# Optimization experiments

Measured on AMD Instinct MI355X. Metric: run time of the kernel, lower is better.

## Reference

```python
import jax, jax.numpy as jnp
import numpy as np

B_, L_, DIN, DM, DS, DR, K = 2, 1024, 1024, 2048, 16, 128, 4


def setup_inputs() -> dict:
    key = jax.random.key(0)
    ks = jax.random.split(key, 10)
    s = lambda k, shape, sc=0.02: (jax.random.normal(k, shape, jnp.float32) * sc)
    A_init = jnp.tile(jnp.arange(1, DS + 1, dtype=jnp.float32)[None, :], (DM, 1))  # (DM, DS)
    return {
        'x_in': jax.random.normal(ks[0], (B_, L_, DIN), jnp.float32),
        'W_in': s(ks[1], (DIN, DM)),
        'W_res': s(ks[2], (DIN, DM)),
        'W_out': s(ks[3], (DM, DIN)),
        'conv_w': s(ks[4], (DM, K), 0.1),   # depthwise conv weight (torch shape (DM,1,K) squeezed)
        'conv_b': jnp.zeros((DM,), jnp.float32),
        'A_log': jnp.log(A_init),
        'D': jnp.ones((DM,), jnp.float32),
        'W_B': s(ks[5], (DM, DS)),
        'W_C': s(ks[6], (DM, DS)),
        'W_dt': s(ks[7], (DM, DR)),
        'dt_w': s(ks[8], (DR, DM)),
        'dt_b': jnp.zeros((DM,), jnp.float32),
    }


def reference(x_in, W_in, W_res, W_out, conv_w, conv_b, A_log, D, W_B, W_C, W_dt, dt_w, dt_b):
    Bb, L, _ = x_in.shape
    x = x_in @ W_in                     # (B, L, DM)
    res = x_in @ W_res                  # (B, L, DM)
    # Causal depthwise conv1d: pad left k-1, truncate to L (matches Conv1d(padding=k-1)[:, :, :L])
    xp = jnp.pad(x, ((0, 0), (K - 1, 0), (0, 0)))
    xc = conv_b
    for i in range(K):
        xc = xc + xp[:, i:i + L, :] * conv_w[:, i]
    xc = jax.nn.silu(xc)                # (B, L, DM)
    # Selective SSM (fused_ssm)
    A = -jnp.exp(A_log)                 # (DM, DS)
    Bp = xc @ W_B                       # (B, L, DS)
    Cp = xc @ W_C                       # (B, L, DS)
    delta = jax.nn.softplus((xc @ W_dt) @ dt_w + dt_b)  # (B, L, DM)
    dA = jnp.exp(delta[..., None] * A)                       # (B, L, DM, DS)
    dBu = delta[..., None] * Bp[:, :, None, :] * xc[..., None]  # (B, L, DM, DS)

    def step(h, inp):
        dA_t, dBu_t, C_t = inp
        h = dA_t * h + dBu_t                         # (B, DM, DS)
        y = jnp.einsum('bdn,bn->bd', h, C_t)         # (B, DM)
        return h, y

    h0 = jnp.zeros((Bb, DM, DS), jnp.float32)
    _, ys = jax.lax.scan(step, h0, (dA.transpose(1, 0, 2, 3), dBu.transpose(1, 0, 2, 3), Cp.transpose(1, 0, 2)))
    y = ys.transpose(1, 0, 2) + D * xc  # (B, L, DM)
    y = y * jax.nn.silu(res)
    return y @ W_out                    # (B, L, DIN)
```

## Files before the change

### kernel.cpp

```cpp
#include <hip/hip_runtime.h>
#include <hip/hip_bf16.h>

constexpr int B_  = 2;
constexpr int L_  = 1024;
constexpr int DIN = 1024;
constexpr int DM  = 2048;
constexpr int DS  = 16;
constexpr int DR  = 128;
constexpr int KC  = 4;
constexpr int M_  = B_ * L_;
constexpr int NP2 = 256;
constexpr int KSLICES = 8;
constexpr int KSL = DM / KSLICES;

constexpr int NC = 64;
constexpr int CL = L_ / NC;
constexpr int S_ = B_ * DM * DS;

typedef __bf16 bf16x8 __attribute__((ext_vector_type(8)));
typedef float  f32x4  __attribute__((ext_vector_type(4)));

__device__ __forceinline__ void gload_lds16(const void* g, void* l) {
    __builtin_amdgcn_global_load_lds(
        (const __attribute__((address_space(1))) void*)g,
        (__attribute__((address_space(3))) void*)l, 16, 0, 0);
}

__device__ __forceinline__ void transpose_block(const float* __restrict__ in,
                                                __bf16* __restrict__ out,
                                                int R, int C, int bx, int by, int t) {
    __shared__ float tile[32][33];
    int tx = t & 31, ty = t >> 5;
    #pragma unroll
    for (int j = 0; j < 32; j += 8)
        tile[ty + j][tx] = in[(size_t)(by * 32 + ty + j) * C + (bx * 32 + tx)];
    __syncthreads();
    #pragma unroll
    for (int j = 0; j < 32; j += 8)
        out[(size_t)(bx * 32 + ty + j) * R + (by * 32 + tx)] = (__bf16)tile[tx][ty + j];
}

__global__ void prep_all(const float* __restrict__ x_in, const float* __restrict__ W_in,
                         const float* __restrict__ W_res, const float* __restrict__ W_out,
                         const float* __restrict__ dt_w,
                         const float* __restrict__ W_B, const float* __restrict__ W_C,
                         const float* __restrict__ W_dt,
                         __bf16* __restrict__ xinB, __bf16* __restrict__ WinT,
                         __bf16* __restrict__ WresT, __bf16* __restrict__ WoutT,
                         __bf16* __restrict__ dtwT, __bf16* __restrict__ projW) {
    int blk = blockIdx.x, t = threadIdx.x;
    if (blk < 8192) {
        int i = blk * 256 + t;
        xinB[i] = (__bf16)x_in[i];
    } else if (blk < 10240) {
        int b = blk - 8192;
        transpose_block(W_in, WinT, DIN, DM, b % 64, b / 64, t);
    } else if (blk < 12288) {
        int b = blk - 10240;
        transpose_block(W_res, WresT, DIN, DM, b % 64, b / 64, t);
    } else if (blk < 14336) {
        int b = blk - 12288;
        transpose_block(W_out, WoutT, DM, DIN, b % 32, b / 32, t);
    } else if (blk < 14592) {
        int b = blk - 14336;
        transpose_block(dt_w, dtwT, DR, DM, b % 64, b / 64, t);
    } else {
        int i = (blk - 14592) * 256 + t;
        int k = i % DM;
        int n = i / DM;
        float v = 0.f;
        if (n < 16)        v = W_B[(size_t)k * DS + n];
        else if (n < 32)   v = W_C[(size_t)k * DS + (n - 16)];
        else if (n < 160)  v = W_dt[(size_t)k * DR + (n - 32)];
        projW[i] = (__bf16)v;
    }
}

__global__ void reduce_split(const float* __restrict__ Ppart, float* __restrict__ Bp,
                             float* __restrict__ Cp, __bf16* __restrict__ dtmpB) {
    int i = blockIdx.x * 256 + threadIdx.x;
    int row = i / 160, c = i % 160;
    float v = 0.f;
    #pragma unroll
    for (int ks = 0; ks < KSLICES; ks++)
        v += Ppart[(size_t)ks * M_ * NP2 + (size_t)row * NP2 + c];
    if (c < 16)       Bp[(size_t)row * DS + c] = v;
    else if (c < 32)  Cp[(size_t)row * DS + (c - 16)] = v;
    else              dtmpB[(size_t)row * DR + (c - 32)] = (__bf16)v;
}

template<int EPI>
__global__ void gemm_tile128(const __bf16* __restrict__ A, const __bf16* __restrict__ BT,
                             float* __restrict__ C0, float* __restrict__ C1,
                             const float* __restrict__ bias, int M, int N, int K,
                             int lda, int ldb) {
    __shared__ __bf16 sA[128 * 32];
    __shared__ __bf16 sB[128 * 32];
    int t = threadIdx.x;
    int lane = t & 63, w = t >> 6;
    int wm = w >> 1, wn = w & 1;
    int m0 = blockIdx.y * 128, n0 = blockIdx.x * 128;
    int kbase = blockIdx.z * K;
    int q = lane >> 4, rr = lane & 15;

    f32x4 acc[4][4] = {};

    int srow = t >> 2;
    int slot = t & 3;

    for (int kt = 0; kt < K; kt += 32) {
        __syncthreads();
        #pragma unroll
        for (int rnd = 0; rnd < 2; rnd++) {
            int row = srow + rnd * 64;
            int gkb = slot ^ ((row >> 1) & 3);
            const __bf16* ga = A  + (size_t)(m0 + row) * lda + kbase + kt + gkb * 8;
            const __bf16* gb = BT + (size_t)(n0 + row) * ldb + kbase + kt + gkb * 8;
            __bf16* la = sA + rnd * 2048 + w * 512;
            __bf16* lb = sB + rnd * 2048 + w * 512;
            gload_lds16(ga, la);
            gload_lds16(gb, lb);
        }
        __syncthreads();

        bf16x8 af[4], bfr[4];
        #pragma unroll
        for (int i = 0; i < 4; i++) {
            int rowA = wm * 64 + i * 16 + rr;
            af[i] = *(const bf16x8*)(sA + rowA * 32 + ((q ^ ((rowA >> 1) & 3)) * 8));
            int rowB = wn * 64 + i * 16 + rr;
            bfr[i] = *(const bf16x8*)(sB + rowB * 32 + ((q ^ ((rowB >> 1) & 3)) * 8));
        }
        #pragma unroll
        for (int i = 0; i < 4; i++)
            #pragma unroll
            for (int j = 0; j < 4; j++)
                acc[i][j] = __builtin_amdgcn_mfma_f32_16x16x32_bf16(af[i], bfr[j], acc[i][j], 0, 0, 0);
    }

    float* Cz = C0 + (size_t)blockIdx.z * M * N;
    #pragma unroll
    for (int i = 0; i < 4; i++) {
        #pragma unroll
        for (int j = 0; j < 4; j++) {
            int col = n0 + wn * 64 + j * 16 + rr;
            #pragma unroll
            for (int jj = 0; jj < 4; jj++) {
                int row = m0 + wm * 64 + i * 16 + q * 4 + jj;
                float v = acc[i][j][jj];
                if (EPI == 0) {
                    Cz[(size_t)row * N + col] = v;
                } else if (EPI == 1) {
                    float z = v + bias[col];
                    C0[(size_t)row * N + col] = (z > 20.f) ? z : log1pf(__expf(z));
                } else {
                    float* o = (col < DM) ? C0 : C1;
                    o[(size_t)row * DM + (col & (DM - 1))] = v;
                }
            }
        }
    }
}

__global__ void conv_silu(const float* __restrict__ x, const float* __restrict__ w,
                          const float* __restrict__ bias, float* __restrict__ xc,
                          __bf16* __restrict__ xcB) {
    int idx = blockIdx.x * 256 + threadIdx.x;
    int d  = idx % DM;
    int bl = idx / DM;
    int l  = bl % L_;
    float acc = bias[d];
    #pragma unroll
    for (int i = 0; i < KC; i++) {
        int li = l - (KC - 1) + i;
        if (li >= 0) acc += x[idx + (i - (KC - 1)) * DM] * w[d * KC + i];
    }
    float v = acc / (1.f + __expf(-acc));
    xc[idx] = v;
    xcB[idx] = (__bf16)v;
}

__global__ void scan_phase1(const float* __restrict__ delta, const float* __restrict__ xc,
                            const float* __restrict__ Bp, const float* __restrict__ A_log,
                            float* __restrict__ aprod, float* __restrict__ cend) {
    int blk = blockIdx.x;
    int c   = blk % NC;
    int rem = blk / NC;
    int dmt = rem % (DM / 256);
    int b   = rem / (DM / 256);
    int t   = threadIdx.x;
    int dm  = dmt * 256 + t;
    int l0  = c * CL;

    __shared__ float sB[CL * DS];
    sB[t] = Bp[((size_t)b * L_ + l0) * DS + t];
    __syncthreads();

    float Aval[DS];
    {
        const f32x4* Ap = (const f32x4*)(A_log + (size_t)dm * DS);
        #pragma unroll
        for (int r4 = 0; r4 < 4; r4++) {
            f32x4 a = Ap[r4];
            #pragma unroll
            for (int q = 0; q < 4; q++) Aval[r4 * 4 + q] = -__expf(a[q]);
        }
    }

    float h[DS], ap[DS];
    #pragma unroll
    for (int i = 0; i < DS; i++) { h[i] = 0.f; ap[i] = 1.f; }

    size_t base = ((size_t)b * L_ + l0) * DM + dm;
    #pragma unroll 4
    for (int j = 0; j < CL; j++) {
        float dl  = delta[base + (size_t)j * DM];
        float xv  = xc[base + (size_t)j * DM];
        float cmn = dl * xv;
        const f32x4* sB4 = (const f32x4*)(sB + j * DS);
        #pragma unroll
        for (int r4 = 0; r4 < 4; r4++) {
            f32x4 bv = sB4[r4];
            #pragma unroll
            for (int q = 0; q < 4; q++) {
                int i = r4 * 4 + q;
                float dA = __expf(dl * Aval[i]);
                ap[i] *= dA;
                h[i] = fmaf(dA, h[i], cmn * bv[q]);
            }
        }
    }

    size_t s = ((size_t)(b * DM + dm)) * DS;
    f32x4* apo = (f32x4*)(aprod + (size_t)c * S_ + s);
    f32x4* ceo = (f32x4*)(cend  + (size_t)c * S_ + s);
    #pragma unroll
    for (int r4 = 0; r4 < 4; r4++) {
        f32x4 va, vh;
        #pragma unroll
        for (int q = 0; q < 4; q++) { va[q] = ap[r4 * 4 + q]; vh[q] = h[r4 * 4 + q]; }
        apo[r4] = va; ceo[r4] = vh;
    }
}

__global__ void scan_phase2(const float* __restrict__ aprod, const float* __restrict__ cend,
                            float* __restrict__ hinit) {
    int u = blockIdx.x * 256 + threadIdx.x;
    float h = 0.f;
    #pragma unroll
    for (int c = 0; c < NC; c++) {
        hinit[(size_t)c * S_ + u] = h;
        h = fmaf(aprod[(size_t)c * S_ + u], h, cend[(size_t)c * S_ + u]);
    }
}

__global__ void scan_phase3(const float* __restrict__ delta, const float* __restrict__ xc,
                            const float* __restrict__ Bp, const float* __restrict__ Cp,
                            const float* __restrict__ res, const float* __restrict__ A_log,
                            const float* __restrict__ Dw, const float* __restrict__ hinit,
                            __bf16* __restrict__ ybar) {
    int blk = blockIdx.x;
    int c   = blk % NC;
    int rem = blk / NC;
    int dmt = rem % (DM / 256);
    int b   = rem / (DM / 256);
    int t   = threadIdx.x;
    int dm  = dmt * 256 + t;
    int l0  = c * CL;

    __shared__ float sB[CL * DS];
    __shared__ float sC[CL * DS];
    sB[t] = Bp[((size_t)b * L_ + l0) * DS + t];
    sC[t] = Cp[((size_t)b * L_ + l0) * DS + t];
    __syncthreads();

    float Aval[DS];
    {
        const f32x4* Ap = (const f32x4*)(A_log + (size_t)dm * DS);
        #pragma unroll
        for (int r4 = 0; r4 < 4; r4++) {
            f32x4 a = Ap[r4];
            #pragma unroll
            for (int q = 0; q < 4; q++) Aval[r4 * 4 + q] = -__expf(a[q]);
        }
    }
    float Dval = Dw[dm];

    float h[DS];
    {
        const f32x4* hi = (const f32x4*)(hinit + (size_t)c * S_ + ((size_t)(b * DM + dm)) * DS);
        #pragma unroll
        for (int r4 = 0; r4 < 4; r4++) {
            f32x4 v = hi[r4];
            #pragma unroll
            for (int q = 0; q < 4; q++) h[r4 * 4 + q] = v[q];
        }
    }

    size_t base = ((size_t)b * L_ + l0) * DM + dm;
    #pragma unroll 4
    for (int j = 0; j < CL; j++) {
        float dl  = delta[base + (size_t)j * DM];
        float xv  = xc[base + (size_t)j * DM];
        float rv  = res[base + (size_t)j * DM];
        float cmn = dl * xv;
        float y = 0.f;
        const f32x4* sB4 = (const f32x4*)(sB + j * DS);
        const f32x4* sC4 = (const f32x4*)(sC + j * DS);
        #pragma unroll
        for (int r4 = 0; r4 < 4; r4++) {
            f32x4 bv = sB4[r4];
            f32x4 cv = sC4[r4];
            #pragma unroll
            for (int q = 0; q < 4; q++) {
                int i = r4 * 4 + q;
                float dA = __expf(dl * Aval[i]);
                h[i] = fmaf(dA, h[i], cmn * bv[q]);
                y = fmaf(h[i], cv[q], y);
            }
        }
        float g = rv / (1.f + __expf(-rv));
        ybar[base + (size_t)j * DM] = (__bf16)((y + Dval * xv) * g);
    }
}

extern "C" void kernel_launch(void* const* d_in, const int* in_sizes, int n_in,
                              void* d_out, int out_size, void* d_ws, size_t ws_size,
                              hipStream_t stream) {
    const float* x_in   = (const float*)d_in[0];
    const float* W_in   = (const float*)d_in[1];
    const float* W_res  = (const float*)d_in[2];
    const float* W_out  = (const float*)d_in[3];
    const float* conv_w = (const float*)d_in[4];
    const float* conv_b = (const float*)d_in[5];
    const float* A_log  = (const float*)d_in[6];
    const float* Dw     = (const float*)d_in[7];
    const float* W_B    = (const float*)d_in[8];
    const float* W_C    = (const float*)d_in[9];
    const float* W_dt   = (const float*)d_in[10];
    const float* dt_w   = (const float*)d_in[11];
    const float* dt_b   = (const float*)d_in[12];

    float* ws_f = (float*)d_ws;
    float* x     = ws_f;
    float* res   = x     + (size_t)M_ * DM;
    float* xc    = res   + (size_t)M_ * DM;
    float* delta = xc    + (size_t)M_ * DM;
    float* Ppart = delta + (size_t)M_ * DM;
    float* Bp    = Ppart + (size_t)KSLICES * M_ * NP2;
    float* Cp    = Bp    + (size_t)M_ * DS;
    float* aprod = Cp    + (size_t)M_ * DS;
    float* cend  = aprod + (size_t)NC * S_;
    float* hinit = cend  + (size_t)NC * S_;
    __bf16* bf_base = (__bf16*)(hinit + (size_t)NC * S_);
    __bf16* ybar  = bf_base;
    __bf16* xinB  = ybar  + (size_t)M_ * DM;
    __bf16* WinT  = xinB  + (size_t)M_ * DIN;
    __bf16* WresT = WinT  + (size_t)DM * DIN;
    __bf16* WoutT = WresT + (size_t)DM * DIN;
    __bf16* xcB   = WoutT + (size_t)DIN * DM;
    __bf16* projW = xcB   + (size_t)M_ * DM;
    __bf16* dtwT  = projW + (size_t)NP2 * DM;
    __bf16* dtmpB = dtwT  + (size_t)DM * DR;

    prep_all<<<16640, 256, 0, stream>>>(x_in, W_in, W_res, W_out, dt_w, W_B, W_C, W_dt,
                                        xinB, WinT, WresT, WoutT, dtwT, projW);

    gemm_tile128<2><<<dim3((2 * DM) / 128, M_ / 128, 1), 256, 0, stream>>>(
        xinB, WinT, x, res, nullptr, M_, 2 * DM, DIN, DIN, DIN);

    conv_silu<<<(M_ * DM) / 256, 256, 0, stream>>>(x, conv_w, conv_b, xc, xcB);

    gemm_tile128<0><<<dim3(NP2 / 128, M_ / 128, KSLICES), 256, 0, stream>>>(
        xcB, projW, Ppart, nullptr, nullptr, M_, NP2, KSL, DM, DM);
    reduce_split<<<(M_ * 160) / 256, 256, 0, stream>>>(Ppart, Bp, Cp, dtmpB);

    gemm_tile128<1><<<dim3(DM / 128, M_ / 128, 1), 256, 0, stream>>>(
        dtmpB, dtwT, delta, nullptr, dt_b, M_, DM, DR, DR, DR);

    int nblk = B_ * (DM / 256) * NC;
    scan_phase1<<<nblk, 256, 0, stream>>>(delta, xc, Bp, A_log, aprod, cend);
    scan_phase2<<<S_ / 256, 256, 0, stream>>>(aprod, cend, hinit);
    scan_phase3<<<nblk, 256, 0, stream>>>(delta, xc, Bp, Cp, res, A_log, Dw, hinit, ybar);

    gemm_tile128<0><<<dim3(DIN / 128, M_ / 128, 1), 256, 0, stream>>>(
        ybar, WoutT, (float*)d_out, nullptr, nullptr, M_, DIN, DM, DM, DM);
}
```

Measured before the change: 292.2 us.

## Store delta, res and xc as bf16 for the scan and split-K the output GEMM

Intermediate activations delta, res and xc are now written and read as bf16 instead of fp32. This halves the memory traffic of the conv, the delta GEMM epilogue and both scan phases. The final output GEMM is split into 8 K-slices, followed by a vectorized reduction kernel, to raise occupancy from only 128 blocks. The trade-offs are reduced precision in the scan inputs (delta and xc at bf16 feed an exp recurrence) and an extra 64MB partial buffer plus its reduction pass.

```diff
diff --git a/kernel.cpp b/kernel.cpp
--- a/kernel.cpp
+++ b/kernel.cpp
@@ -12,6 +12,8 @@
 constexpr int NP2 = 256;
 constexpr int KSLICES = 8;
 constexpr int KSL = DM / KSLICES;
+constexpr int OSLICES = 8;
+constexpr int OSL = DM / OSLICES;
 
 constexpr int NC = 64;
 constexpr int CL = L_ / NC;
@@ -89,9 +91,18 @@
     else              dtmpB[(size_t)row * DR + (c - 32)] = (__bf16)v;
 }
 
+__global__ void reduce_out(const float* __restrict__ Opart, float* __restrict__ out) {
+    int i = blockIdx.x * 256 + threadIdx.x;
+    f32x4 s = ((const f32x4*)Opart)[i];
+    #pragma unroll
+    for (int ks = 1; ks < OSLICES; ks++)
+        s += ((const f32x4*)(Opart + (size_t)ks * M_ * DIN))[i];
+    ((f32x4*)out)[i] = s;
+}
+
 template<int EPI>
 __global__ void gemm_tile128(const __bf16* __restrict__ A, const __bf16* __restrict__ BT,
-                             float* __restrict__ C0, float* __restrict__ C1,
+                             float* __restrict__ Cf, __bf16* __restrict__ Cb,
                              const float* __restrict__ bias, int M, int N, int K,
                              int lda, int ldb) {
     __shared__ __bf16 sA[128 * 32];
@@ -138,7 +149,7 @@
                 acc[i][j] = __builtin_amdgcn_mfma_f32_16x16x32_bf16(af[i], bfr[j], acc[i][j], 0, 0, 0);
     }
 
-    float* Cz = C0 + (size_t)blockIdx.z * M * N;
+    float* Cz = Cf + (size_t)blockIdx.z * M * N;
     #pragma unroll
     for (int i = 0; i < 4; i++) {
         #pragma unroll
@@ -152,10 +163,10 @@
                     Cz[(size_t)row * N + col] = v;
                 } else if (EPI == 1) {
                     float z = v + bias[col];
-                    C0[(size_t)row * N + col] = (z > 20.f) ? z : log1pf(__expf(z));
+                    Cb[(size_t)row * N + col] = (__bf16)((z > 20.f) ? z : log1pf(__expf(z)));
                 } else {
-                    float* o = (col < DM) ? C0 : C1;
-                    o[(size_t)row * DM + (col & (DM - 1))] = v;
+                    if (col < DM) Cf[(size_t)row * DM + col] = v;
+                    else          Cb[(size_t)row * DM + (col - DM)] = (__bf16)v;
                 }
             }
         }
@@ -163,8 +174,7 @@
 }
 
 __global__ void conv_silu(const float* __restrict__ x, const float* __restrict__ w,
-                          const float* __restrict__ bias, float* __restrict__ xc,
-                          __bf16* __restrict__ xcB) {
+                          const float* __restrict__ bias, __bf16* __restrict__ xcB) {
     int idx = blockIdx.x * 256 + threadIdx.x;
     int d  = idx % DM;
     int bl = idx / DM;
@@ -176,11 +186,10 @@
         if (li >= 0) acc += x[idx + (i - (KC - 1)) * DM] * w[d * KC + i];
     }
     float v = acc / (1.f + __expf(-acc));
-    xc[idx] = v;
     xcB[idx] = (__bf16)v;
 }
 
-__global__ void scan_phase1(const float* __restrict__ delta, const float* __restrict__ xc,
+__global__ void scan_phase1(const __bf16* __restrict__ delta, const __bf16* __restrict__ xc,
                             const float* __restrict__ Bp, const float* __restrict__ A_log,
                             float* __restrict__ aprod, float* __restrict__ cend) {
     int blk = blockIdx.x;
@@ -214,8 +223,8 @@
     size_t base = ((size_t)b * L_ + l0) * DM + dm;
     #pragma unroll 4
     for (int j = 0; j < CL; j++) {
-        float dl  = delta[base + (size_t)j * DM];
-        float xv  = xc[base + (size_t)j * DM];
+        float dl  = (float)delta[base + (size_t)j * DM];
+        float xv  = (float)xc[base + (size_t)j * DM];
         float cmn = dl * xv;
         const f32x4* sB4 = (const f32x4*)(sB + j * DS);
         #pragma unroll
@@ -254,9 +263,9 @@
     }
 }
 
-__global__ void scan_phase3(const float* __restrict__ delta, const float* __restrict__ xc,
+__global__ void scan_phase3(const __bf16* __restrict__ delta, const __bf16* __restrict__ xc,
                             const float* __restrict__ Bp, const float* __restrict__ Cp,
-                            const float* __restrict__ res, const float* __restrict__ A_log,
+                            const __bf16* __restrict__ res, const float* __restrict__ A_log,
                             const float* __restrict__ Dw, const float* __restrict__ hinit,
                             __bf16* __restrict__ ybar) {
     int blk = blockIdx.x;
@@ -300,9 +309,9 @@
     size_t base = ((size_t)b * L_ + l0) * DM + dm;
     #pragma unroll 4
     for (int j = 0; j < CL; j++) {
-        float dl  = delta[base + (size_t)j * DM];
-        float xv  = xc[base + (size_t)j * DM];
-        float rv  = res[base + (size_t)j * DM];
+        float dl  = (float)delta[base + (size_t)j * DM];
+        float xv  = (float)xc[base + (size_t)j * DM];
+        float rv  = (float)res[base + (size_t)j * DM];
         float cmn = dl * xv;
         float y = 0.f;
         const f32x4* sB4 = (const f32x4*)(sB + j * DS);
@@ -343,46 +352,47 @@
 
     float* ws_f = (float*)d_ws;
     float* x     = ws_f;
-    float* res   = x     + (size_t)M_ * DM;
-    float* xc    = res   + (size_t)M_ * DM;
-    float* delta = xc    + (size_t)M_ * DM;
-    float* Ppart = delta + (size_t)M_ * DM;
-    float* Bp    = Ppart + (size_t)KSLICES * M_ * NP2;
+    float* Ppart = x     + (size_t)M_ * DM;
+    float* Opart = Ppart + (size_t)KSLICES * M_ * NP2;
+    float* Bp    = Opart + (size_t)OSLICES * M_ * DIN;
     float* Cp    = Bp    + (size_t)M_ * DS;
     float* aprod = Cp    + (size_t)M_ * DS;
     float* cend  = aprod + (size_t)NC * S_;
     float* hinit = cend  + (size_t)NC * S_;
     __bf16* bf_base = (__bf16*)(hinit + (size_t)NC * S_);
-    __bf16* ybar  = bf_base;
-    __bf16* xinB  = ybar  + (size_t)M_ * DM;
-    __bf16* WinT  = xinB  + (size_t)M_ * DIN;
-    __bf16* WresT = WinT  + (size_t)DM * DIN;
-    __bf16* WoutT = WresT + (size_t)DM * DIN;
-    __bf16* xcB   = WoutT + (size_t)DIN * DM;
-    __bf16* projW = xcB   + (size_t)M_ * DM;
-    __bf16* dtwT  = projW + (size_t)NP2 * DM;
-    __bf16* dtmpB = dtwT  + (size_t)DM * DR;
+    __bf16* ybar   = bf_base;
+    __bf16* xinB   = ybar   + (size_t)M_ * DM;
+    __bf16* WinT   = xinB   + (size_t)M_ * DIN;
+    __bf16* WresT  = WinT   + (size_t)DM * DIN;
+    __bf16* WoutT  = WresT  + (size_t)DM * DIN;
+    __bf16* xcB    = WoutT  + (size_t)DIN * DM;
+    __bf16* projW  = xcB    + (size_t)M_ * DM;
+    __bf16* dtwT   = projW  + (size_t)NP2 * DM;
+    __bf16* dtmpB  = dtwT   + (size_t)DM * DR;
+    __bf16* deltaB = dtmpB  + (size_t)M_ * DR;
+    __bf16* resB   = deltaB + (size_t)M_ * DM;
 
     prep_all<<<16640, 256, 0, stream>>>(x_in, W_in, W_res, W_out, dt_w, W_B, W_C, W_dt,
                                         xinB, WinT, WresT, WoutT, dtwT, projW);
 
     gemm_tile128<2><<<dim3((2 * DM) / 128, M_ / 128, 1), 256, 0, stream>>>(
-        xinB, WinT, x, res, nullptr, M_, 2 * DM, DIN, DIN, DIN);
-
-    conv_silu<<<(M_ * DM) / 256, 256, 0, stream>>>(x, conv_w, conv_b, xc, xcB);
+        xinB, WinT, x, resB, nullptr, M_, 2 * DM, DIN, DIN, DIN);
+
+    conv_silu<<<(M_ * DM) / 256, 256, 0, stream>>>(x, conv_w, conv_b, xcB);
 
     gemm_tile128<0><<<dim3(NP2 / 128, M_ / 128, KSLICES), 256, 0, stream>>>(
         xcB, projW, Ppart, nullptr, nullptr, M_, NP2, KSL, DM, DM);
     reduce_split<<<(M_ * 160) / 256, 256, 0, stream>>>(Ppart, Bp, Cp, dtmpB);
 
     gemm_tile128<1><<<dim3(DM / 128, M_ / 128, 1), 256, 0, stream>>>(
-        dtmpB, dtwT, delta, nullptr, dt_b, M_, DM, DR, DR, DR);
+        dtmpB, dtwT, nullptr, deltaB, dt_b, M_, DM, DR, DR, DR);
 
     int nblk = B_ * (DM / 256) * NC;
-    scan_phase1<<<nblk, 256, 0, stream>>>(delta, xc, Bp, A_log, aprod, cend);
+    scan_phase1<<<nblk, 256, 0, stream>>>(deltaB, xcB, Bp, A_log, aprod, cend);
     scan_phase2<<<S_ / 256, 256, 0, stream>>>(aprod, cend, hinit);
-    scan_phase3<<<nblk, 256, 0, stream>>>(delta, xc, Bp, Cp, res, A_log, Dw, hinit, ybar);
-
-    gemm_tile128<0><<<dim3(DIN / 128, M_ / 128, 1), 256, 0, stream>>>(
-        ybar, WoutT, (float*)d_out, nullptr, nullptr, M_, DIN, DM, DM, DM);
-}
+    scan_phase3<<<nblk, 256, 0, stream>>>(deltaB, xcB, Bp, Cp, resB, A_log, Dw, hinit, ybar);
+
+    gemm_tile128<0><<<dim3(DIN / 128, M_ / 128, OSLICES), 256, 0, stream>>>(
+        ybar, WoutT, Opart, nullptr, nullptr, M_, DIN, OSL, DM, DM);
+    reduce_out<<<(M_ * DIN) / 1024, 256, 0, stream>>>(Opart, (float*)d_out);
+}
```

New measurement: 295.0 us. Within noise of the previous version (+0.9%).
